# Optimization experiments

Hardware: AMD Instinct MI355X
Metric: run time of the kernel (lower is better)

The kernel has to match this reference:

```python
import jax, jax.numpy as jnp
import numpy as np

D_MODEL = 4096
N_TYPES = 6  # fixed event_types list in the module


def setup_inputs() -> dict:
    key = jax.random.key(0)
    ks = jax.random.split(key, 7)
    E, B, d = 131072, 16384, D_MODEL
    return {
        "event_type": jax.random.randint(ks[0], (E,), 0, N_TYPES),
        "confidence": jax.random.uniform(ks[1], (E,), jnp.float32),
        "location": jax.random.uniform(ks[2], (E, 2), jnp.float32) * jnp.array([640.0, 480.0], jnp.float32),
        "batch_idx": jax.random.randint(ks[3], (E,), 0, B),
        "batch_size": B,
        "type_emb": jax.random.normal(ks[4], (N_TYPES, d // 4), jnp.float32),
        "W1": jax.random.normal(ks[5], (d // 2, d // 4 + 3), jnp.float32) / np.sqrt(d // 4 + 3).astype(np.float32),
        "b1": jnp.zeros((d // 2,), jnp.float32),
        "W2": jax.random.normal(ks[6], (d, d // 2), jnp.float32) / np.sqrt(d // 2).astype(np.float32),
        "b2": jnp.zeros((d,), jnp.float32),
    }


def reference(event_type, confidence, location, batch_idx, batch_size, type_emb, W1, b1, W2, b2):
    E = confidence.shape[0]
    B = batch_size
    # per-batch-slot max confidence (empty slots -> -inf)
    seg_max = jax.ops.segment_max(confidence, batch_idx, num_segments=B)
    is_top = confidence == seg_max[batch_idx]
    # first event attaining the max (matches torch's max-over-list semantics)
    cand = jnp.where(is_top, jnp.arange(E), E)
    top_idx = jnp.full((B,), E, dtype=cand.dtype).at[batch_idx].min(cand)
    has_event = top_idx < E
    safe_idx = jnp.where(has_event, top_idx, 0)

    emb = type_emb[event_type[safe_idx]]                 # [B, d/4]
    c = confidence[safe_idx][:, None]                    # [B, 1]
    loc = location[safe_idx] / jnp.array([640.0, 480.0], jnp.float32)  # [B, 2]
    feats = jnp.concatenate([emb, c, loc], axis=-1)      # [B, d/4 + 3]

    h = jax.nn.relu(feats @ W1.T + b1)                   # [B, d/2]
    out = h @ W2.T + b2                                  # [B, d]
    return jnp.where(has_event[:, None], out, jnp.zeros((), out.dtype))
```

## Files before the change

### kernel.cpp

```cpp
#include <hip/hip_runtime.h>
#include <hip/hip_bf16.h>

#define NT 6
#define BM 256
#define BN 128
#define BK 32
#define ASLOT (BM * BK)
#define BSLOT (BN * BK)
#define SLOT  (ASLOT + BSLOT)

typedef __attribute__((ext_vector_type(4))) float f32x4;
typedef __attribute__((ext_vector_type(8))) short bf16x8;

__device__ __forceinline__ short f2bf(float f) {
    __hip_bfloat16 h = __float2bfloat16(f);
    return (short)__builtin_bit_cast(unsigned short, h);
}

__global__ void k_segmax(const float* __restrict__ conf,
                         const int* __restrict__ bidx,
                         unsigned long long* __restrict__ packed, int E) {
    int i = blockIdx.x * blockDim.x + threadIdx.x;
    if (i >= E) return;
    unsigned cb = __float_as_uint(conf[i]);
    unsigned long long p = ((unsigned long long)cb << 32) | (unsigned)(~(unsigned)i);
    atomicMax(&packed[bidx[i]], p);
}

__global__ void k_base(const float* __restrict__ emb, const float* __restrict__ W1,
                       const float* __restrict__ b1, float* __restrict__ base,
                       float* __restrict__ vecs, int d2, int d4) {
    int gw = (blockIdx.x * blockDim.x + threadIdx.x) >> 6;
    int lane = threadIdx.x & 63;
    int t = gw / d2, n = gw % d2;
    const float* e = emb + (size_t)t * d4;
    const float* w = W1 + (size_t)n * (d4 + 3);
    float s = 0.f;
    for (int k = lane; k < d4; k += 64) s += e[k] * w[k];
#pragma unroll
    for (int m = 32; m; m >>= 1) s += __shfl_xor(s, m);
    if (lane == 0) {
        base[gw] = s + b1[n];
        if (t == 0) {
            vecs[n]          = w[d4];
            vecs[d2 + n]     = w[d4 + 1];
            vecs[2 * d2 + n] = w[d4 + 2];
        }
    }
}

__global__ void k_w2cast(const float* __restrict__ W2, short* __restrict__ W2b, long n) {
    long i = ((long)blockIdx.x * blockDim.x + threadIdx.x) * 8;
    if (i >= n) return;
    bf16x8 v;
#pragma unroll
    for (int j = 0; j < 8; ++j) v[j] = f2bf(W2[i + j]);
    *(bf16x8*)(W2b + i) = v;
}

__global__ void k_h(const unsigned long long* __restrict__ packed,
                    const int* __restrict__ etype, const float* __restrict__ loc,
                    const float* __restrict__ base, const float* __restrict__ vecs,
                    float* __restrict__ mask, short* __restrict__ h, int d2) {
    int b = blockIdx.x;
    int tid = threadIdx.x;
    unsigned long long p = packed[b];
    bool has = (p != 0ULL);
    float conf = 0.f, lx = 0.f, ly = 0.f;
    int t = 0;
    if (has) {
        unsigned idx = ~(unsigned)(p & 0xFFFFFFFFu);
        conf = __uint_as_float((unsigned)(p >> 32));
        t  = etype[idx];
        lx = loc[2 * (size_t)idx]     * (1.0f / 640.0f);
        ly = loc[2 * (size_t)idx + 1] * (1.0f / 480.0f);
    }
    if (tid == 0) mask[b] = has ? 1.0f : 0.0f;
    const float* bs = base + (size_t)t * d2;
    const float* cv = vecs;
    const float* xv = vecs + d2;
    const float* yv = vecs + 2 * d2;
    int n0 = tid * 8;
    bf16x8 v;
#pragma unroll
    for (int j = 0; j < 8; ++j) {
        int n = n0 + j;
        float g = bs[n] + conf * cv[n] + lx * xv[n] + ly * yv[n];
        g = fmaxf(g, 0.f);
        v[j] = has ? f2bf(g) : (short)0;
    }
    *(bf16x8*)(h + (size_t)b * d2 + n0) = v;
}


#define GLL(src, dst) __builtin_amdgcn_global_load_lds(                      \
    (const __attribute__((address_space(1))) void*)(src),                    \
    (__attribute__((address_space(3))) void*)(dst), 16, 0, 0)

#define STAGE3(slotp) do {                                                   \
    GLL(pa0, (slotp) + dA0); GLL(pa1, (slotp) + dA1);                        \
    GLL(pb0, (slotp) + dB0);                                                 \
    pa0 += BK; pa1 += BK; pb0 += BK; } while (0)

__global__ __launch_bounds__(512, 4)
void k_gemm(const short* __restrict__ A, const short* __restrict__ Bm,
            const float* __restrict__ b2, const float* __restrict__ mask,
            float* __restrict__ C, int M, int N, int K, int nbn) {
    __shared__ __align__(16) short lds[3 * SLOT];

    int tid = threadIdx.x;
    int lane = tid & 63;
    int wave = tid >> 6;
    int wr = wave >> 1, wc = wave & 1;

    int bid = blockIdx.x;
    int wg = (bid & 7) * ((int)gridDim.x >> 3) + (bid >> 3);
    int bm = wg / nbn, bn = wg % nbn;
    int row0 = bm * BM, col0 = bn * BN;

    int srow = tid >> 2;
    int chunkL = (tid & 3) ^ ((srow >> 1) & 3);
    const short* pa0 = A + (size_t)(row0 + srow) * K + chunkL * 8;
    const short* pa1 = pa0 + (size_t)128 * K;
    const short* pb0 = Bm + (size_t)(col0 + srow) * K + chunkL * 8;
    int dA0 = tid * 8, dA1 = 4096 + tid * 8, dB0 = 8192 + tid * 8;

    int frow = lane & 15, fk = lane >> 4;
    int cp = fk ^ ((frow >> 1) & 3);
    int aoff = (wr * 64 + frow) * 32 + cp * 8;
    int boff = 8192 + (wc * 64 + frow) * 32 + cp * 8;

    f32x4 acc[4][4] = {};
    bf16x8 af[4], bv[4];

    int KT = K / BK;

    STAGE3(lds + 0 * SLOT);
    STAGE3(lds + 1 * SLOT);
    asm volatile("s_waitcnt vmcnt(3)" ::: "memory");
    __builtin_amdgcn_s_barrier();

    int cs = 0, ws = 2;
#pragma unroll 1
    for (int t = 0; t < KT; ++t) {
        const short* slotr = lds + cs * SLOT;
        if (++cs == 3) cs = 0;
#pragma unroll
        for (int m = 0; m < 4; ++m)
            af[m] = *(const bf16x8*)(slotr + aoff + m * 512);
#pragma unroll
        for (int n = 0; n < 4; ++n)
            bv[n] = *(const bf16x8*)(slotr + boff + n * 512);
        if (t < KT - 2) {
            short* slotw = lds + ws * SLOT;
            if (++ws == 3) ws = 0;
            STAGE3(slotw);
        }
        __builtin_amdgcn_s_setprio(1);
#pragma unroll
        for (int m = 0; m < 4; ++m)
#pragma unroll
            for (int n = 0; n < 4; ++n)
                acc[m][n] = __builtin_amdgcn_mfma_f32_16x16x32_bf16(
                    af[m], bv[n], acc[m][n], 0, 0, 0);
        __builtin_amdgcn_s_setprio(0);
        if (t < KT - 1) {
            if (t < KT - 2) asm volatile("s_waitcnt vmcnt(3)" ::: "memory");
            else            asm volatile("s_waitcnt vmcnt(0)" ::: "memory");
            __builtin_amdgcn_s_barrier();
        }
    }

#pragma unroll
    for (int m = 0; m < 4; ++m) {
        int rbase = row0 + wr * 64 + m * 16 + (lane >> 4) * 4;
#pragma unroll
        for (int j = 0; j < 4; ++j) {
            int r = rbase + j;
            float mk = mask[r];
#pragma unroll
            for (int n = 0; n < 4; ++n) {
                int c = col0 + wc * 64 + n * 16 + frow;
                C[(size_t)r * N + c] = (acc[m][n][j] + b2[c]) * mk;
            }
        }
    }
}

extern "C" void kernel_launch(void* const* d_in, const int* in_sizes, int n_in,
                              void* d_out, int out_size, void* d_ws, size_t ws_size,
                              hipStream_t stream) {
    const int* etype   = (const int*)d_in[0];
    const float* conf  = (const float*)d_in[1];
    const float* loc   = (const float*)d_in[2];
    const int* bidx    = (const int*)d_in[3];
    const float* emb   = (const float*)d_in[5];
    const float* W1    = (const float*)d_in[6];
    const float* b1    = (const float*)d_in[7];
    const float* W2    = (const float*)d_in[8];
    const float* b2    = (const float*)d_in[9];
    float* out = (float*)d_out;

    int E  = in_sizes[0];
    int d2 = in_sizes[7];
    int d  = in_sizes[9];
    int d4 = in_sizes[5] / NT;
    int B  = out_size / d;

    char* ws = (char*)d_ws;
    unsigned long long* packed = (unsigned long long*)ws;
    float* mask = (float*)(ws + (size_t)B * 8);
    float* base = mask + B;
    float* vecs = base + NT * d2;
    short* w2b  = (short*)(vecs + 3 * d2);
    short* h    = w2b + (size_t)d * d2;

    hipMemsetAsync(packed, 0, (size_t)B * 8, stream);
    k_segmax<<<(E + 255) / 256, 256, 0, stream>>>(conf, bidx, packed, E);
    k_base<<<(NT * d2) / 4, 256, 0, stream>>>(emb, W1, b1, base, vecs, d2, d4);
    long nw2 = (long)d * d2;
    k_w2cast<<<(int)(nw2 / 8 / 256), 256, 0, stream>>>(W2, w2b, nw2);
    k_h<<<B, 256, 0, stream>>>(packed, etype, loc, base, vecs, mask, h, d2);
    int nbm = B / BM, nbn = d / BN;
    k_gemm<<<dim3(nbm * nbn), dim3(512), 0, stream>>>(h, w2b, b2, mask, out, B, d, d2, nbn);
}
```

Baseline: 347.7 us.

## Enlarge GEMM tile to 256x256 with 32x32x16 MFMA and 4-stage pipeline

```diff
diff --git a/kernel.cpp b/kernel.cpp
--- a/kernel.cpp
+++ b/kernel.cpp
@@ -3,13 +3,12 @@
 
 #define NT 6
 #define BM 256
-#define BN 128
+#define BN 256
 #define BK 32
-#define ASLOT (BM * BK)
-#define BSLOT (BN * BK)
-#define SLOT  (ASLOT + BSLOT)
+#define SLOT 16384
 
 typedef __attribute__((ext_vector_type(4))) float f32x4;
+typedef __attribute__((ext_vector_type(16))) float f32x16;
 typedef __attribute__((ext_vector_type(8))) short bf16x8;
 
 __device__ __forceinline__ short f2bf(float f) {
@@ -97,21 +96,21 @@
     (const __attribute__((address_space(1))) void*)(src),                    \
     (__attribute__((address_space(3))) void*)(dst), 16, 0, 0)
 
-#define STAGE3(slotp) do {                                                   \
+#define STAGE4(slotp) do {                                                   \
     GLL(pa0, (slotp) + dA0); GLL(pa1, (slotp) + dA1);                        \
-    GLL(pb0, (slotp) + dB0);                                                 \
-    pa0 += BK; pa1 += BK; pb0 += BK; } while (0)
-
-__global__ __launch_bounds__(512, 4)
+    GLL(pb0, (slotp) + dB0); GLL(pb1, (slotp) + dB1);                        \
+    pa0 += BK; pa1 += BK; pb0 += BK; pb1 += BK; } while (0)
+
+__global__ __launch_bounds__(512, 2)
 void k_gemm(const short* __restrict__ A, const short* __restrict__ Bm,
             const float* __restrict__ b2, const float* __restrict__ mask,
             float* __restrict__ C, int M, int N, int K, int nbn) {
-    __shared__ __align__(16) short lds[3 * SLOT];
+    __shared__ __align__(16) short lds[4 * SLOT];
 
     int tid = threadIdx.x;
     int lane = tid & 63;
     int wave = tid >> 6;
-    int wr = wave >> 1, wc = wave & 1;
+    int wr = wave >> 2, wc = wave & 3;
 
     int bid = blockIdx.x;
     int wg = (bid & 7) * ((int)gridDim.x >> 3) + (bid >> 3);
@@ -123,65 +122,82 @@
     const short* pa0 = A + (size_t)(row0 + srow) * K + chunkL * 8;
     const short* pa1 = pa0 + (size_t)128 * K;
     const short* pb0 = Bm + (size_t)(col0 + srow) * K + chunkL * 8;
-    int dA0 = tid * 8, dA1 = 4096 + tid * 8, dB0 = 8192 + tid * 8;
-
-    int frow = lane & 15, fk = lane >> 4;
-    int cp = fk ^ ((frow >> 1) & 3);
-    int aoff = (wr * 64 + frow) * 32 + cp * 8;
-    int boff = 8192 + (wc * 64 + frow) * 32 + cp * 8;
-
-    f32x4 acc[4][4] = {};
-    bf16x8 af[4], bv[4];
+    const short* pb1 = pb0 + (size_t)128 * K;
+    int dA0 = tid * 8, dA1 = 4096 + tid * 8;
+    int dB0 = 8192 + tid * 8, dB1 = 12288 + tid * 8;
+
+    int l31 = lane & 31, kh = lane >> 5;
+    int g = (l31 >> 1) & 3;
+    int cp0 = kh ^ g;
+    int cp1 = (2 + kh) ^ g;
+    int aoff = (wr * 128 + l31) * 32;
+    int boff = 8192 + (wc * 64 + l31) * 32;
+
+    f32x16 acc[4][2] = {};
+    bf16x8 af[4][2], bf_[2][2];
 
     int KT = K / BK;
 
-    STAGE3(lds + 0 * SLOT);
-    STAGE3(lds + 1 * SLOT);
-    asm volatile("s_waitcnt vmcnt(3)" ::: "memory");
+    STAGE4(lds + 0 * SLOT);
+    STAGE4(lds + 1 * SLOT);
+    STAGE4(lds + 2 * SLOT);
+    asm volatile("s_waitcnt vmcnt(8)" ::: "memory");
     __builtin_amdgcn_s_barrier();
 
-    int cs = 0, ws = 2;
 #pragma unroll 1
     for (int t = 0; t < KT; ++t) {
-        const short* slotr = lds + cs * SLOT;
-        if (++cs == 3) cs = 0;
+        const short* sr = lds + (t & 3) * SLOT;
+        bf_[0][0] = *(const bf16x8*)(sr + boff + cp0 * 8);
+        bf_[0][1] = *(const bf16x8*)(sr + boff + cp1 * 8);
+        bf_[1][0] = *(const bf16x8*)(sr + boff + 1024 + cp0 * 8);
+        bf_[1][1] = *(const bf16x8*)(sr + boff + 1024 + cp1 * 8);
+        af[0][0] = *(const bf16x8*)(sr + aoff + cp0 * 8);
+        af[0][1] = *(const bf16x8*)(sr + aoff + cp1 * 8);
+        af[1][0] = *(const bf16x8*)(sr + aoff + 1024 + cp0 * 8);
+        af[1][1] = *(const bf16x8*)(sr + aoff + 1024 + cp1 * 8);
+        if (t < KT - 3) {
+            short* sw = lds + ((t + 3) & 3) * SLOT;
+            STAGE4(sw);
+        }
+        af[2][0] = *(const bf16x8*)(sr + aoff + 2048 + cp0 * 8);
+        af[2][1] = *(const bf16x8*)(sr + aoff + 2048 + cp1 * 8);
+        af[3][0] = *(const bf16x8*)(sr + aoff + 3072 + cp0 * 8);
+        af[3][1] = *(const bf16x8*)(sr + aoff + 3072 + cp1 * 8);
+
+        __builtin_amdgcn_s_setprio(1);
 #pragma unroll
         for (int m = 0; m < 4; ++m)
-            af[m] = *(const bf16x8*)(slotr + aoff + m * 512);
-#pragma unroll
-        for (int n = 0; n < 4; ++n)
-            bv[n] = *(const bf16x8*)(slotr + boff + n * 512);
-        if (t < KT - 2) {
-            short* slotw = lds + ws * SLOT;
-            if (++ws == 3) ws = 0;
-            STAGE3(slotw);
-        }
-        __builtin_amdgcn_s_setprio(1);
-#pragma unroll
-        for (int m = 0; m < 4; ++m)
-#pragma unroll
-            for (int n = 0; n < 4; ++n)
-                acc[m][n] = __builtin_amdgcn_mfma_f32_16x16x32_bf16(
-                    af[m], bv[n], acc[m][n], 0, 0, 0);
+#pragma unroll
+            for (int n2 = 0; n2 < 2; ++n2) {
+                acc[m][n2] = __builtin_amdgcn_mfma_f32_32x32x16_bf16(
+                    af[m][0], bf_[n2][0], acc[m][n2], 0, 0, 0);
+                acc[m][n2] = __builtin_amdgcn_mfma_f32_32x32x16_bf16(
+                    af[m][1], bf_[n2][1], acc[m][n2], 0, 0, 0);
+            }
         __builtin_amdgcn_s_setprio(0);
+
         if (t < KT - 1) {
-            if (t < KT - 2) asm volatile("s_waitcnt vmcnt(3)" ::: "memory");
-            else            asm volatile("s_waitcnt vmcnt(0)" ::: "memory");
+            if (t < KT - 3)       asm volatile("s_waitcnt vmcnt(8)" ::: "memory");
+            else if (t == KT - 3) asm volatile("s_waitcnt vmcnt(4)" ::: "memory");
+            else                  asm volatile("s_waitcnt vmcnt(0)" ::: "memory");
             __builtin_amdgcn_s_barrier();
         }
     }
 
 #pragma unroll
     for (int m = 0; m < 4; ++m) {
-        int rbase = row0 + wr * 64 + m * 16 + (lane >> 4) * 4;
-#pragma unroll
-        for (int j = 0; j < 4; ++j) {
-            int r = rbase + j;
-            float mk = mask[r];
-#pragma unroll
-            for (int n = 0; n < 4; ++n) {
-                int c = col0 + wc * 64 + n * 16 + frow;
-                C[(size_t)r * N + c] = (acc[m][n][j] + b2[c]) * mk;
+        int rb = row0 + wr * 128 + m * 32 + 4 * kh;
+#pragma unroll
+        for (int q = 0; q < 4; ++q) {
+#pragma unroll
+            for (int j = 0; j < 4; ++j) {
+                int r = rb + 8 * q + j;
+                float mk = mask[r];
+#pragma unroll
+                for (int n2 = 0; n2 < 2; ++n2) {
+                    int c = col0 + wc * 64 + n2 * 32 + l31;
+                    C[(size_t)r * N + c] = (acc[m][n2][q * 4 + j] + b2[c]) * mk;
+                }
             }
         }
     }
```

Measured after the change: 350.9 us. No clear change (+0.9%).
